# Performance work log

Measured on AMD Instinct MI355X. Metric: run time of the kernel, lower is better.

## Reference

```python
import jax, jax.numpy as jnp
import numpy as np

B, T, C = 4, 1024, 1024          # batch, seq, d_model
E = 8                             # num_local_experts
TOP_K = 2                         # num_experts_per_tok
H = 512                           # expert_dim
HS = 2048                         # shared_expert_dim


def setup_inputs() -> dict:
    key = jax.random.key(0)
    ks = jax.random.split(key, 7)
    std = 0.02
    return {
        "x": jax.random.normal(ks[0], (B, T, C), dtype=jnp.float32),
        "router_w": jax.random.normal(ks[1], (E, C), dtype=jnp.float32) * std,
        "gate_up_w": jax.random.normal(ks[2], (E, C, 2 * H), dtype=jnp.float32) * std,
        "down_w": jax.random.normal(ks[3], (E, H, C), dtype=jnp.float32) * std,
        "shared_gate_w": jax.random.normal(ks[4], (HS, C), dtype=jnp.float32) * std,
        "shared_up_w": jax.random.normal(ks[5], (HS, C), dtype=jnp.float32) * std,
        "shared_down_w": jax.random.normal(ks[6], (C, HS), dtype=jnp.float32) * std,
    }


def reference(x, router_w, gate_up_w, down_w, shared_gate_w, shared_up_w, shared_down_w):
    b, t, c = x.shape
    n = b * t
    xf = x.reshape(n, c)

    # --- router: topk logits, sigmoid gates ---
    logits = xf @ router_w.T                                  # [N, E]
    top_vals, top_idx = jax.lax.top_k(logits, TOP_K)          # [N, K]
    gates = jax.nn.sigmoid(top_vals)                          # [N, K]

    # combine weights [N, E]: gate where expert selected, 0 otherwise
    # (scatter-add matches torch scatter_add_; topk indices are distinct)
    combine = jnp.zeros((n, E), dtype=x.dtype)
    combine = combine.at[jnp.arange(n)[:, None], top_idx].add(gates)

    # --- experts: dense SwiGLU per expert, masked combine ---
    # mathematically identical to per-pair gather+bmm+scatter_add in the
    # original (unselected experts get weight 0)
    gu = jnp.einsum('nc,ecH->enH', xf, gate_up_w)             # [E, N, 2H]
    gate, up = jnp.split(gu, 2, axis=-1)
    hidden = jax.nn.silu(gate) * up                           # [E, N, H]
    expert_out = jnp.einsum('enh,ehc->enc', hidden, down_w)   # [E, N, C]
    moe_out = jnp.einsum('ne,enc->nc', combine, expert_out)   # [N, C]

    # --- shared expert (SwiGLU) ---
    shared = (jax.nn.silu(xf @ shared_gate_w.T) * (xf @ shared_up_w.T)) @ shared_down_w.T

    return (moe_out + shared).reshape(b, t, c)
```

## Files before the change

### kernel.cpp

```cpp
#include <hip/hip_runtime.h>
#include <stdint.h>

typedef unsigned short u16;
typedef u16 u16x4 __attribute__((ext_vector_type(4)));
typedef u16 u16x8 __attribute__((ext_vector_type(8)));
typedef float f32x4 __attribute__((ext_vector_type(4)));
typedef __bf16 bf16x8 __attribute__((ext_vector_type(8)));

#define N_TOK 4096
#define C_DIM 1024
#define E_NUM 8
#define H_DIM 512
#define HS_DIM 2048
#define NPAIR (N_TOK * 2)

__device__ __forceinline__ u16 f2b(float f) {
    uint32_t u = __builtin_bit_cast(uint32_t, f);
    uint32_t r = (u + 0x7FFFu + ((u >> 16) & 1u)) >> 16;
    return (u16)r;
}
__device__ __forceinline__ float b2f(u16 h) {
    uint32_t u = ((uint32_t)h) << 16;
    return __builtin_bit_cast(float, u);
}

__global__ void k_convert(const float* __restrict__ in, u16* __restrict__ out, int n4) {
    int i = blockIdx.x * blockDim.x + threadIdx.x;
    if (i >= n4) return;
    f32x4 v = ((const f32x4*)in)[i];
    u16x4 o;
    o.x = f2b(v.x); o.y = f2b(v.y); o.z = f2b(v.z); o.w = f2b(v.w);
    ((u16x4*)out)[i] = o;
}

__global__ void k_convT(const float* __restrict__ in, u16* __restrict__ out, int R, int S) {
    __shared__ float t[32][33];
    int z = blockIdx.z;
    const float* inz = in + (size_t)z * R * S;
    u16* outz = out + (size_t)z * R * S;
    int s0 = blockIdx.x * 32, r0 = blockIdx.y * 32;
    int tx = threadIdx.x, ty = threadIdx.y;
#pragma unroll
    for (int i = 0; i < 4; i++)
        t[ty + 8 * i][tx] = inz[(size_t)(r0 + ty + 8 * i) * S + s0 + tx];
    __syncthreads();
#pragma unroll
    for (int i = 0; i < 4; i++)
        outz[(size_t)(s0 + ty + 8 * i) * R + r0 + tx] = f2b(t[tx][ty + 8 * i]);
}

__global__ __launch_bounds__(256) void k_router(const float* __restrict__ x,
                                                const float* __restrict__ rw,
                                                int* __restrict__ topidx,
                                                float* __restrict__ gatev) {
    __shared__ float srw[E_NUM * C_DIM];
    int tid = threadIdx.x;
#pragma unroll
    for (int i = 0; i < E_NUM * C_DIM / 4 / 256; i++)
        ((f32x4*)srw)[tid + 256 * i] = ((const f32x4*)rw)[tid + 256 * i];
    __syncthreads();

    int wave = tid >> 6, lane = tid & 63;
    int wid = blockIdx.x * 4 + wave;
#pragma unroll
    for (int it = 0; it < 4; it++) {
        int n = wid + 1024 * it;
        const f32x4* xr = (const f32x4*)(x + (size_t)n * C_DIM);
        float acc[E_NUM];
#pragma unroll
        for (int e = 0; e < E_NUM; e++) acc[e] = 0.f;
#pragma unroll
        for (int c4 = 0; c4 < 4; c4++) {
            int idx = lane + 64 * c4;
            f32x4 xv = xr[idx];
#pragma unroll
            for (int e = 0; e < E_NUM; e++) {
                f32x4 wv = ((const f32x4*)srw)[e * 256 + idx];
                acc[e] += xv.x * wv.x + xv.y * wv.y + xv.z * wv.z + xv.w * wv.w;
            }
        }
#pragma unroll
        for (int e = 0; e < E_NUM; e++)
#pragma unroll
            for (int m = 32; m >= 1; m >>= 1) acc[e] += __shfl_xor(acc[e], m);
        if (lane == 0) {
            int i1 = 0; float v1 = acc[0];
#pragma unroll
            for (int e = 1; e < E_NUM; e++) if (acc[e] > v1) { v1 = acc[e]; i1 = e; }
            int i2 = -1; float v2 = -1e30f;
#pragma unroll
            for (int e = 0; e < E_NUM; e++) if (e != i1 && acc[e] > v2) { v2 = acc[e]; i2 = e; }
            topidx[n * 2] = i1; topidx[n * 2 + 1] = i2;
            gatev[n * 2] = 1.f / (1.f + __expf(-v1));
            gatev[n * 2 + 1] = 1.f / (1.f + __expf(-v2));
        }
    }
}

__global__ __launch_bounds__(1024) void k_build(const int* __restrict__ topidx,
                                                const float* __restrict__ gatev,
                                                int* __restrict__ offs,
                                                int* __restrict__ pairlist,
                                                float* __restrict__ gate_g) {
    __shared__ int wcnt[16][E_NUM];
    __shared__ int wbase[16][E_NUM];
    int tid = threadIdx.x, wave = tid >> 6, lane = tid & 63;

    int cnt[E_NUM];
#pragma unroll
    for (int e = 0; e < E_NUM; e++) cnt[e] = 0;
#pragma unroll
    for (int i = 0; i < 8; i++) {
        int idx = topidx[wave * 512 + i * 64 + lane];
#pragma unroll
        for (int e = 0; e < E_NUM; e++) {
            unsigned long long m = __ballot(idx == e);
            cnt[e] += __popcll(m);
        }
    }
    if (lane == 0)
#pragma unroll
        for (int e = 0; e < E_NUM; e++) wcnt[wave][e] = cnt[e];
    __syncthreads();

    if (tid == 0) {
        int o = 0;
        for (int e = 0; e < E_NUM; e++) {
            offs[e] = o;
            int r = o;
            for (int w = 0; w < 16; w++) { wbase[w][e] = r; r += wcnt[w][e]; }
            o = r;
        }
        offs[E_NUM] = o;
    }
    __syncthreads();

    int run[E_NUM];
#pragma unroll
    for (int e = 0; e < E_NUM; e++) run[e] = wbase[wave][e];
#pragma unroll
    for (int i = 0; i < 8; i++) {
        int gi = wave * 512 + i * 64 + lane;
        int idx = topidx[gi];
        float gv = gatev[gi];
        int pos = 0;
#pragma unroll
        for (int e = 0; e < E_NUM; e++) {
            unsigned long long m = __ballot(idx == e);
            unsigned long long below = m & ((1ull << lane) - 1ull);
            if (idx == e) pos = run[e] + __popcll(below);
            run[e] += __popcll(m);
        }
        pairlist[pos] = gi;
        gate_g[pos] = gv;
    }
}

template <bool GATHER_A, bool SCATTER_C, bool OUT_BF16, bool ADD_PAIRS>
__global__ __launch_bounds__(256) void k_gemm(
    const u16* __restrict__ A, const u16* __restrict__ B, void* __restrict__ Cout,
    const u16* __restrict__ pairbuf, const int* __restrict__ offs,
    const int* __restrict__ pairlist, int M, int N, int K) {
    int e = blockIdx.z;
    int base = 0, cnt = M;
    if (offs) { base = offs[e]; cnt = offs[e + 1] - base; }
    int m0 = blockIdx.y * 128;
    if (m0 >= cnt) return;
    int n0 = blockIdx.x * 128;
    const u16* Bp = B + (size_t)e * N * K;

    __shared__ __align__(16) u16 lA[128 * 32];
    __shared__ __align__(16) u16 lB[128 * 32];

    int tid = threadIdx.x;
    int w = tid >> 6, lane = tid & 63;
    int wr = w >> 1, wc = w & 1;

    int srow = lane >> 2;
    int scol = (lane & 3) * 8;

    size_t arow_off[2];
#pragma unroll
    for (int i = 0; i < 2; i++) {
        int r = (2 * w + i) * 16 + srow;
        int rr = m0 + r; if (rr > cnt - 1) rr = cnt - 1;
        long grow;
        if (GATHER_A) grow = (long)(pairlist[base + rr] >> 1);
        else          grow = (long)(base + rr);
        arow_off[i] = (size_t)grow * K;
    }

    f32x4 acc[4][4];
#pragma unroll
    for (int i = 0; i < 4; i++)
#pragma unroll
        for (int j = 0; j < 4; j++) acc[i][j] = f32x4{0.f, 0.f, 0.f, 0.f};

    for (int k0 = 0; k0 < K; k0 += 32) {
#pragma unroll
        for (int i = 0; i < 2; i++) {
            int r = (2 * w + i) * 16 + srow;
            const u16* gA = A + arow_off[i] + k0 + scol;
            const u16* gB = Bp + (size_t)(n0 + r) * K + k0 + scol;
            __builtin_amdgcn_global_load_lds(
                (const __attribute__((address_space(1))) void*)gA,
                (__attribute__((address_space(3))) void*)&lA[(2 * w + i) * 16 * 32], 16, 0, 0);
            __builtin_amdgcn_global_load_lds(
                (const __attribute__((address_space(1))) void*)gB,
                (__attribute__((address_space(3))) void*)&lB[(2 * w + i) * 16 * 32], 16, 0, 0);
        }
        __syncthreads();
        bf16x8 af[4], bfr[4];
#pragma unroll
        for (int m = 0; m < 4; m++) {
            int row = wr * 64 + m * 16 + (lane & 15);
            af[m] = *(const bf16x8*)&lA[row * 32 + (lane >> 4) * 8];
        }
#pragma unroll
        for (int n = 0; n < 4; n++) {
            int row = wc * 64 + n * 16 + (lane & 15);
            bfr[n] = *(const bf16x8*)&lB[row * 32 + (lane >> 4) * 8];
        }
#pragma unroll
        for (int m = 0; m < 4; m++)
#pragma unroll
            for (int n = 0; n < 4; n++)
                acc[m][n] = __builtin_amdgcn_mfma_f32_16x16x32_bf16(af[m], bfr[n], acc[m][n], 0, 0, 0);
        __syncthreads();
    }

#pragma unroll
    for (int m = 0; m < 4; m++) {
#pragma unroll
        for (int j = 0; j < 4; j++) {
            int rloc = wr * 64 + m * 16 + (lane >> 4) * 4 + j;
            if (m0 + rloc >= cnt) continue;
            long crow;
            if (SCATTER_C) crow = pairlist[base + m0 + rloc];
            else           crow = base + m0 + rloc;
#pragma unroll
            for (int n = 0; n < 4; n++) {
                int col = n0 + wc * 64 + n * 16 + (lane & 15);
                float v = acc[m][n][j];
                if (ADD_PAIRS) {
                    v += b2f(pairbuf[(size_t)(2 * crow) * N + col]) +
                         b2f(pairbuf[(size_t)(2 * crow + 1) * N + col]);
                    ((float*)Cout)[(size_t)crow * N + col] = v;
                } else if (OUT_BF16) {
                    ((u16*)Cout)[(size_t)crow * N + col] = f2b(v);
                } else {
                    ((float*)Cout)[(size_t)crow * N + col] = v;
                }
            }
        }
    }
}

__global__ void k_swiglu_e(const u16* __restrict__ gu, const float* __restrict__ gate_g,
                           u16* __restrict__ hid) {
    int i = blockIdx.x * blockDim.x + threadIdx.x;
    if (i >= NPAIR * 64) return;
    int p = i >> 6;
    int h0 = (i & 63) * 8;
    float gs = gate_g[p];
    u16x8 gv = *(const u16x8*)(gu + (size_t)p * 1024 + h0);
    u16x8 uv = *(const u16x8*)(gu + (size_t)p * 1024 + 512 + h0);
    u16x8 ov;
#pragma unroll
    for (int j = 0; j < 8; j++) {
        float g = b2f(gv[j]), u = b2f(uv[j]);
        float s = g / (1.f + __expf(-g));
        ov[j] = f2b(gs * s * u);
    }
    *(u16x8*)(hid + (size_t)p * 512 + h0) = ov;
}

__global__ void k_swiglu_s(const u16* __restrict__ gu, u16* __restrict__ hid) {
    int i = blockIdx.x * blockDim.x + threadIdx.x;
    if (i >= N_TOK * 256) return;
    int p = i >> 8;
    int h0 = (i & 255) * 8;
    u16x8 gv = *(const u16x8*)(gu + (size_t)p * 4096 + h0);
    u16x8 uv = *(const u16x8*)(gu + (size_t)p * 4096 + 2048 + h0);
    u16x8 ov;
#pragma unroll
    for (int j = 0; j < 8; j++) {
        float g = b2f(gv[j]), u = b2f(uv[j]);
        float s = g / (1.f + __expf(-g));
        ov[j] = f2b(s * u);
    }
    *(u16x8*)(hid + (size_t)p * 2048 + h0) = ov;
}

extern "C" void kernel_launch(void* const* d_in, const int* in_sizes, int n_in,
                              void* d_out, int out_size, void* d_ws, size_t ws_size,
                              hipStream_t stream) {
    const float* x   = (const float*)d_in[0];
    const float* rw  = (const float*)d_in[1];
    const float* guw = (const float*)d_in[2];
    const float* dnw = (const float*)d_in[3];
    const float* sgw = (const float*)d_in[4];
    const float* suw = (const float*)d_in[5];
    const float* sdw = (const float*)d_in[6];
    float* out = (float*)d_out;
    char* ws = (char*)d_ws;

    u16* xb        = (u16*)(ws + 0);
    u16* w_gu      = (u16*)(ws + 8388608);
    u16* guout     = (u16*)(ws + 25165824);
    u16* sharedgu  = (u16*)(ws + 8388608);
    u16* w_dn      = (u16*)(ws + 41943040);
    u16* hidden    = (u16*)(ws + 50331648);
    u16* sharedhid = (u16*)(ws + 41943040);
    u16* w_sgu     = (u16*)(ws + 58720256);
    u16* w_sd      = (u16*)(ws + 67108864);
    u16* pairout   = (u16*)(ws + 71303168);
    int*   topidx   = (int*)(ws + 88080384);
    float* gatev    = (float*)(ws + 88080384 + 32768);
    int*   pairlist = (int*)(ws + 88080384 + 65536);
    float* gate_g   = (float*)(ws + 88080384 + 98304);
    int*   offs     = (int*)(ws + 88080384 + 131072);

    k_convert<<<4096, 256, 0, stream>>>(x, xb, 1048576);
    k_convert<<<2048, 256, 0, stream>>>(sgw, w_sgu, 524288);
    k_convert<<<2048, 256, 0, stream>>>(suw, w_sgu + 2048 * 1024, 524288);
    k_convert<<<2048, 256, 0, stream>>>(sdw, w_sd, 524288);
    dim3 tb(32, 8);
    k_convT<<<dim3(32, 32, 8), tb, 0, stream>>>(guw, w_gu, 1024, 1024);
    k_convT<<<dim3(32, 16, 8), tb, 0, stream>>>(dnw, w_dn, 512, 1024);

    k_router<<<256, 256, 0, stream>>>(x, rw, topidx, gatev);
    k_build<<<1, 1024, 0, stream>>>(topidx, gatev, offs, pairlist, gate_g);

    k_gemm<true, false, true, false><<<dim3(8, 32, 8), 256, 0, stream>>>(
        xb, w_gu, guout, nullptr, offs, pairlist, 0, 1024, 1024);
    k_swiglu_e<<<2048, 256, 0, stream>>>(guout, gate_g, hidden);
    k_gemm<false, true, true, false><<<dim3(8, 32, 8), 256, 0, stream>>>(
        hidden, w_dn, pairout, nullptr, offs, pairlist, 0, 1024, 512);

    k_gemm<false, false, true, false><<<dim3(32, 32, 1), 256, 0, stream>>>(
        xb, w_sgu, sharedgu, nullptr, nullptr, nullptr, 4096, 4096, 1024);
    k_swiglu_s<<<4096, 256, 0, stream>>>(sharedgu, sharedhid);
    k_gemm<false, false, false, true><<<dim3(8, 32, 1), 256, 0, stream>>>(
        sharedhid, w_sd, out, pairout, nullptr, nullptr, 4096, 1024, 2048);
}
```

Measured before the change: 339.2 us.

## Add 256x256 tiled 8-wave GEMM with async LDS loads for shared gate/up projection

Result: slower. 362.8 us (+7.0%).

```diff
diff --git a/kernel.cpp b/kernel.cpp
--- a/kernel.cpp
+++ b/kernel.cpp
@@ -254,6 +254,142 @@
             }
         }
     }
+}
+
+__device__ __forceinline__ void mfma16q(f32x4 (&accq)[4][2], bf16x8 (&afr)[4][2],
+                                        bf16x8 (&bf)[2][2]) {
+    __builtin_amdgcn_s_setprio(1);
+#pragma unroll
+    for (int mf = 0; mf < 4; mf++)
+#pragma unroll
+        for (int nf = 0; nf < 2; nf++)
+#pragma unroll
+            for (int ks = 0; ks < 2; ks++)
+                accq[mf][nf] = __builtin_amdgcn_mfma_f32_16x16x32_bf16(
+                    afr[mf][ks], bf[nf][ks], accq[mf][nf], 0, 0, 0);
+    __builtin_amdgcn_s_setprio(0);
+}
+
+__global__ __launch_bounds__(512, 1) void k_gemm8(const u16* __restrict__ A,
+                                                  const u16* __restrict__ B,
+                                                  u16* __restrict__ C,
+                                                  int M, int N, int K, int gx) {
+    __shared__ __align__(16) u16 smem[65536];
+
+    int nwg = gridDim.x;
+    int cpx = nwg >> 3;
+    int bid = blockIdx.x;
+    int sz = (bid & 7) * cpx + (bid >> 3);
+    int bx = sz % gx, by = sz / gx;
+    int m0 = by * 256, n0 = bx * 256;
+
+    int tid = threadIdx.x, w = tid >> 6, lane = tid & 63;
+    int nkt = K >> 6;
+
+    int l2 = lane ^ (((lane >> 5) & 1) << 1);
+    int colh = (l2 & 7) * 8;
+    int r0s = w * 8 + (l2 >> 3);
+    const u16* a_src[2][2];
+    const u16* b_src[2][2];
+#pragma unroll
+    for (int h = 0; h < 2; h++)
+#pragma unroll
+        for (int i = 0; i < 2; i++) {
+            a_src[h][i] = A + (size_t)(m0 + h * 128 + i * 64 + r0s) * K + colh;
+            b_src[h][i] = B + (size_t)(n0 + h * 128 + i * 64 + r0s) * K + colh;
+        }
+    int sdst = w * 512 + lane * 8;
+
+    int sxor = (lane & 4) << 2;
+    int arow = (w >> 2) * 64 + (lane & 15);
+    int brow = (w & 3) * 32 + (lane & 15);
+    int kcol = (lane >> 4) * 8;
+
+    f32x4 acc[2][2][4][2];
+#pragma unroll
+    for (int a = 0; a < 2; a++)
+#pragma unroll
+        for (int b = 0; b < 2; b++)
+#pragma unroll
+            for (int c = 0; c < 4; c++)
+#pragma unroll
+                for (int d = 0; d < 2; d++) acc[a][b][c][d] = f32x4{0.f, 0.f, 0.f, 0.f};
+    bf16x8 afr[4][2], bfr0[2][2], bfr1[2][2];
+
+#define GLD(srcp, dsto) __builtin_amdgcn_global_load_lds( \
+        (const __attribute__((address_space(1))) void*)(srcp), \
+        (__attribute__((address_space(3))) void*)&smem[dsto], 16, 0, 0)
+#define STG_A(D, H, KO) do { GLD(a_src[H][0] + (KO), ((D)*2+(H))*8192 + sdst); \
+                             GLD(a_src[H][1] + (KO), ((D)*2+(H))*8192 + 4096 + sdst); } while (0)
+#define STG_B(D, H, KO) do { GLD(b_src[H][0] + (KO), 32768 + ((D)*2+(H))*8192 + sdst); \
+                             GLD(b_src[H][1] + (KO), 32768 + ((D)*2+(H))*8192 + 4096 + sdst); } while (0)
+#define LDA(D, H) do { _Pragma("unroll") \
+    for (int mf = 0; mf < 4; mf++) { _Pragma("unroll") \
+        for (int ks = 0; ks < 2; ks++) \
+            afr[mf][ks] = *(const bf16x8*)&smem[((((D)*2+(H))*8192) + (arow + mf*16)*64 + ks*32 + kcol) ^ sxor]; } } while (0)
+#define LDB(BF, D, H) do { _Pragma("unroll") \
+    for (int nf = 0; nf < 2; nf++) { _Pragma("unroll") \
+        for (int ks = 0; ks < 2; ks++) \
+            BF[nf][ks] = *(const bf16x8*)&smem[(32768 + (((D)*2+(H))*8192) + (brow + nf*16)*64 + ks*32 + kcol) ^ sxor]; } } while (0)
+#define VMCNT4 asm volatile("s_waitcnt vmcnt(4)" ::: "memory")
+#define VMCNT0 asm volatile("s_waitcnt vmcnt(0)" ::: "memory")
+#define LGKM0 asm volatile("s_waitcnt lgkmcnt(0)" ::: "memory")
+#define BAR __builtin_amdgcn_s_barrier()
+#define SCB __builtin_amdgcn_sched_barrier(0)
+
+    STG_A(0, 0, 0); STG_A(0, 1, 0); STG_B(0, 0, 0); STG_B(0, 1, 0);
+    VMCNT0; BAR;
+
+    for (int t = 0; t < nkt; t += 2) {
+        int ko1 = (t + 1) << 6;
+        int ko2 = (t + 2) << 6;
+        bool st = (t + 2) < nkt;
+        LDA(0, 0); LDB(bfr0, 0, 0); STG_B(1, 0, ko1); VMCNT4; BAR; LGKM0; SCB;
+        mfma16q(acc[0][0], afr, bfr0); SCB; BAR;
+        LDB(bfr1, 0, 1);            STG_A(1, 0, ko1); VMCNT4; BAR; LGKM0; SCB;
+        mfma16q(acc[0][1], afr, bfr1); SCB; BAR;
+        LDA(0, 1);                  STG_B(1, 1, ko1); VMCNT4; BAR; LGKM0; SCB;
+        mfma16q(acc[1][1], afr, bfr1); SCB; BAR;
+                                    STG_A(1, 1, ko1); VMCNT4; BAR; LGKM0; SCB;
+        mfma16q(acc[1][0], afr, bfr0); SCB; BAR;
+        LDA(1, 0); LDB(bfr0, 1, 0);
+        if (st) { STG_B(0, 0, ko2); VMCNT4; } else { VMCNT0; }
+        BAR; LGKM0; SCB; mfma16q(acc[0][0], afr, bfr0); SCB; BAR;
+        LDB(bfr1, 1, 1);
+        if (st) { STG_A(0, 0, ko2); VMCNT4; }
+        BAR; LGKM0; SCB; mfma16q(acc[0][1], afr, bfr1); SCB; BAR;
+        LDA(1, 1);
+        if (st) { STG_B(0, 1, ko2); VMCNT4; }
+        BAR; LGKM0; SCB; mfma16q(acc[1][1], afr, bfr1); SCB; BAR;
+        if (st) { STG_A(0, 1, ko2); VMCNT4; }
+        BAR; LGKM0; SCB; mfma16q(acc[1][0], afr, bfr0); SCB; BAR;
+    }
+
+#undef GLD
+#undef STG_A
+#undef STG_B
+#undef LDA
+#undef LDB
+#undef VMCNT4
+#undef VMCNT0
+#undef LGKM0
+#undef BAR
+#undef SCB
+
+#pragma unroll
+    for (int mh = 0; mh < 2; mh++)
+#pragma unroll
+        for (int nh = 0; nh < 2; nh++)
+#pragma unroll
+            for (int mf = 0; mf < 4; mf++)
+#pragma unroll
+                for (int nf = 0; nf < 2; nf++) {
+                    int r = m0 + mh * 128 + (w >> 2) * 64 + mf * 16 + ((lane >> 4) << 2);
+                    int c = n0 + nh * 128 + (w & 3) * 32 + nf * 16 + (lane & 15);
+#pragma unroll
+                    for (int j = 0; j < 4; j++)
+                        C[(size_t)(r + j) * N + c] = f2b(acc[mh][nh][mf][nf][j]);
+                }
 }
 
 __global__ void k_swiglu_e(const u16* __restrict__ gu, const float* __restrict__ gate_g,
@@ -338,8 +474,7 @@
     k_gemm<false, true, true, false><<<dim3(8, 32, 8), 256, 0, stream>>>(
         hidden, w_dn, pairout, nullptr, offs, pairlist, 0, 1024, 512);
 
-    k_gemm<false, false, true, false><<<dim3(32, 32, 1), 256, 0, stream>>>(
-        xb, w_sgu, sharedgu, nullptr, nullptr, nullptr, 4096, 4096, 1024);
+    k_gemm8<<<256, 512, 0, stream>>>(xb, w_sgu, sharedgu, 4096, 4096, 1024, 16);
     k_swiglu_s<<<4096, 256, 0, stream>>>(sharedgu, sharedhid);
     k_gemm<false, false, false, true><<<dim3(8, 32, 1), 256, 0, stream>>>(
         sharedhid, w_sd, out, pairout, nullptr, nullptr, 4096, 1024, 2048);
```
